# Kernel tuning notes

Measured on AMD Instinct MI355X. Metric: run time of the kernel, lower is better.

Reference implementation:

```python
import jax, jax.numpy as jnp
import numpy as np
from jax import lax

# Model hyperparameters (from module source: D_state=2, Expand=1; mamba-ssm defaults)
B_, C_, H_, W_ = 16, 128, 96, 96
D_MODEL = C_
D_INNER = 1 * D_MODEL          # expand = 1
D_STATE = 2
DT_RANK = (D_MODEL + 15) // 16  # ceil(d_model/16) = 8
D_CONV = 4
OUT_C = 128
LN_EPS = 1e-5


def setup_inputs() -> dict:
    key = jax.random.key(0)
    ks = jax.random.split(key, 10)
    s = 0.02
    x = jax.random.normal(ks[0], (B_, C_, H_, W_), dtype=jnp.float32)
    in_proj_w = jax.random.normal(ks[1], (2 * D_INNER, D_MODEL), dtype=jnp.float32) * s
    conv_w = jax.random.normal(ks[2], (D_INNER, 1, D_CONV), dtype=jnp.float32) * s
    conv_b = jnp.zeros((D_INNER,), dtype=jnp.float32)
    x_proj_w = jax.random.normal(ks[3], (DT_RANK + 2 * D_STATE, D_INNER), dtype=jnp.float32) * s
    dt_proj_w = jax.random.normal(ks[4], (D_INNER, DT_RANK), dtype=jnp.float32) * s
    # softplus^{-1}(0.01) so initial dt ~ 0.01 (standard mamba init)
    dt_proj_b = jnp.full((D_INNER,), float(np.log(np.expm1(0.01))), dtype=jnp.float32)
    A_log = jnp.log(jnp.broadcast_to(jnp.arange(1, D_STATE + 1, dtype=jnp.float32), (D_INNER, D_STATE)))
    D_param = jnp.ones((D_INNER,), dtype=jnp.float32)
    out_proj_w = jax.random.normal(ks[5], (OUT_C, D_INNER), dtype=jnp.float32) * s
    ln_gamma = jnp.ones((OUT_C,), dtype=jnp.float32)
    ln_beta = jnp.zeros((OUT_C,), dtype=jnp.float32)
    return {
        "x": x, "in_proj_w": in_proj_w, "conv_w": conv_w, "conv_b": conv_b,
        "x_proj_w": x_proj_w, "dt_proj_w": dt_proj_w, "dt_proj_b": dt_proj_b,
        "A_log": A_log, "D_param": D_param, "out_proj_w": out_proj_w,
        "ln_gamma": ln_gamma, "ln_beta": ln_beta,
    }


def _ssm_cha(x, in_proj_w, conv_w, conv_b, x_proj_w, dt_proj_w, dt_proj_b,
             A_log, D_param, out_proj_w, ln_gamma, ln_beta):
    b, c, h, w = x.shape
    L = h * w
    tokens = x.transpose(0, 2, 3, 1).reshape(b, L, c)  # [b, L, d_model]

    # in_proj -> (x_in, z)
    xz = jnp.einsum("bld,ed->ble", tokens, in_proj_w)  # [b, L, 2*d_inner]
    x_in, z = jnp.split(xz, 2, axis=-1)

    # causal depthwise conv1d over L, then SiLU
    xc = x_in.transpose(0, 2, 1)  # [b, d_inner, L]
    xc = lax.conv_general_dilated(
        xc, conv_w, window_strides=(1,), padding=[(D_CONV - 1, 0)],
        dimension_numbers=("NCH", "OIH", "NCH"), feature_group_count=D_INNER,
    ) + conv_b[None, :, None]
    x_in = jax.nn.silu(xc).transpose(0, 2, 1)  # [b, L, d_inner]

    # x_proj -> (dt, B, C)
    x_dbl = jnp.einsum("bld,ed->ble", x_in, x_proj_w)
    dt = x_dbl[..., :DT_RANK]
    Bc = x_dbl[..., DT_RANK:DT_RANK + D_STATE]         # [b, L, n]
    Cc = x_dbl[..., DT_RANK + D_STATE:]                # [b, L, n]
    dt = jax.nn.softplus(jnp.einsum("blr,dr->bld", dt, dt_proj_w) + dt_proj_b)

    # selective scan (diagonal A) via associative scan over L
    A = -jnp.exp(A_log)                                # [d_inner, n]
    dA = jnp.exp(dt[..., None] * A)                    # [b, L, d_inner, n]
    dBx = dt[..., None] * Bc[:, :, None, :] * x_in[..., None]

    def combine(e1, e2):
        a1, b1 = e1
        a2, b2 = e2
        return a1 * a2, a2 * b1 + b2

    _, hstate = lax.associative_scan(combine, (dA, dBx), axis=1)  # [b, L, d, n]
    y = jnp.sum(hstate * Cc[:, :, None, :], axis=-1) + D_param * x_in  # [b, L, d]

    y = y * jax.nn.silu(z)
    out = jnp.einsum("bld,od->blo", y, out_proj_w)     # [b, L, out_c]

    # LayerNorm over out_c
    mu = jnp.mean(out, axis=-1, keepdims=True)
    var = jnp.mean(jnp.square(out - mu), axis=-1, keepdims=True)
    out = (out - mu) * lax.rsqrt(var + LN_EPS) * ln_gamma + ln_beta

    return out.reshape(b, h, w, OUT_C).transpose(0, 3, 1, 2)


def reference(x, in_proj_w, conv_w, conv_b, x_proj_w, dt_proj_w, dt_proj_b,
              A_log, D_param, out_proj_w, ln_gamma, ln_beta):
    return _ssm_cha(x, in_proj_w, conv_w, conv_b, x_proj_w, dt_proj_w, dt_proj_b,
                    A_log, D_param, out_proj_w, ln_gamma, ln_beta)
```

## Files before the change

### kernel.cpp

```cpp
#include <hip/hip_runtime.h>
#include <hip/hip_bf16.h>

#define B_N 16
#define L_N 9216
#define LT64 144

typedef __attribute__((ext_vector_type(8))) short short8;
typedef __attribute__((ext_vector_type(4))) float floatx4;

__device__ __forceinline__ float bfu(unsigned short u) {
  return __uint_as_float(((unsigned int)u) << 16);
}
__device__ __forceinline__ unsigned short fbf(float f) {
  __hip_bfloat16 h = __float2bfloat16(f);
  return *(unsigned short*)&h;
}

__global__ __launch_bounds__(256) void k_prep(const float* __restrict__ w1,
                                              const float* __restrict__ w2,
                                              __hip_bfloat16* __restrict__ w1bt,
                                              __hip_bfloat16* __restrict__ w2bt) {
  int i = blockIdx.x * 256 + threadIdx.x;
  if (i < 256 * 128) w1bt[i] = __float2bfloat16(w1[i]);
  if (i < 128 * 128) w2bt[i] = __float2bfloat16(w2[i]);
}

__global__ __launch_bounds__(256) void k_xt(const float* __restrict__ x,
                                            __hip_bfloat16* __restrict__ xt) {
  __shared__ float xs[128][65];
  int blk = blockIdx.x, b = blk / LT64, lt = blk % LT64, l0 = lt * 64;
  int t = threadIdx.x;
  const float* xb = x + (size_t)b * 128 * L_N;
#pragma unroll
  for (int i = 0; i < 8; ++i) {
    int idx = t + i * 256;
    int c = idx >> 4, f4 = idx & 15;
    float4 v = *(const float4*)(xb + (size_t)c * L_N + l0 + f4 * 4);
    xs[c][f4 * 4 + 0] = v.x; xs[c][f4 * 4 + 1] = v.y;
    xs[c][f4 * 4 + 2] = v.z; xs[c][f4 * 4 + 3] = v.w;
  }
  __syncthreads();
  __hip_bfloat16* xtb = xt + ((size_t)b * L_N + l0) * 128;
#pragma unroll
  for (int i = 0; i < 16; ++i) {
    int idx = t + i * 256;
    int cp = idx & 63, l = idx >> 6;
    __hip_bfloat162 u;
    u.x = __float2bfloat16(xs[2 * cp][l]);
    u.y = __float2bfloat16(xs[2 * cp + 1][l]);
    *(__hip_bfloat162*)(xtb + (size_t)l * 128 + 2 * cp) = u;
  }
}

__global__ __launch_bounds__(256) void k_inproj_conv(
    const __hip_bfloat16* __restrict__ xt, const __hip_bfloat16* __restrict__ w1bt,
    const float* __restrict__ cw, const float* __restrict__ cb,
    const float* __restrict__ xpw,
    __hip_bfloat16* __restrict__ xinb, __hip_bfloat16* __restrict__ zb,
    float* __restrict__ xdblT) {
  __shared__ __align__(16) char smem[16384];
  __hip_bfloat16* xs = (__hip_bfloat16*)smem;
  float (*red)[12][64] = (float(*)[12][64])smem;
  __shared__ float cvs[128][68];
  int blk = blockIdx.x, b = blk / LT64, lt = blk % LT64, l0 = lt * 64;
  int t = threadIdx.x;
  const __hip_bfloat16* src = xt + ((size_t)b * L_N + l0) * 128;
#pragma unroll
  for (int i = 0; i < 4; ++i) {
    int idx = t + i * 256;
    int row = idx >> 4, ch = idx & 15;
    uint4 v = *(const uint4*)(src + idx * 8);
    *(uint4*)&xs[row * 128 + ((ch ^ (row & 7)) * 8)] = v;
  }
  int lane = t & 63, wv = t >> 6;
  int col = lane & 15, quad = lane >> 4;
  int e0 = wv * 64;
  short8 afr[4][4];
  const __hip_bfloat16* wb = w1bt + (size_t)(e0 + col) * 128 + quad * 8;
#pragma unroll
  for (int mi = 0; mi < 4; ++mi)
#pragma unroll
    for (int ks = 0; ks < 4; ++ks)
      afr[mi][ks] = *(const short8*)(wb + mi * 16 * 128 + ks * 32);
  floatx4 vzero = {0.f, 0.f, 0.f, 0.f};
  floatx4 acc[4][4];
#pragma unroll
  for (int mi = 0; mi < 4; ++mi)
#pragma unroll
    for (int ni = 0; ni < 4; ++ni) acc[mi][ni] = vzero;
  __syncthreads();
#pragma unroll
  for (int ks = 0; ks < 4; ++ks) {
    short8 bfr[4];
#pragma unroll
    for (int ni = 0; ni < 4; ++ni) {
      int row = ni * 16 + col;
      bfr[ni] = *(const short8*)&xs[row * 128 + (((ks * 4 + quad) ^ (row & 7)) * 8)];
    }
#pragma unroll
    for (int mi = 0; mi < 4; ++mi)
#pragma unroll
      for (int ni = 0; ni < 4; ++ni)
        acc[mi][ni] = __builtin_amdgcn_mfma_f32_16x16x32_bf16(afr[mi][ks], bfr[ni], acc[mi][ni], 0, 0, 0);
  }
  if (t < 128) {
    float s0 = 0.f, s1 = 0.f, s2 = 0.f;
    if (lt > 0) {
      const __hip_bfloat16* wr = w1bt + (size_t)t * 128;
      const __hip_bfloat16* x0r = xt + ((size_t)b * L_N + l0 - 3) * 128;
#pragma unroll
      for (int c8 = 0; c8 < 16; ++c8) {
        short8 wc = *(const short8*)(wr + c8 * 8);
        short8 xa = *(const short8*)(x0r + c8 * 8);
        short8 xb2 = *(const short8*)(x0r + 128 + c8 * 8);
        short8 xc = *(const short8*)(x0r + 256 + c8 * 8);
#pragma unroll
        for (int e = 0; e < 8; ++e) {
          float wf = bfu((unsigned short)wc[e]);
          s0 += wf * bfu((unsigned short)xa[e]);
          s1 += wf * bfu((unsigned short)xb2[e]);
          s2 += wf * bfu((unsigned short)xc[e]);
        }
      }
    }
    cvs[t][0] = s0; cvs[t][1] = s1; cvs[t][2] = s2;
  }
  if (wv < 2) {
#pragma unroll
    for (int mi = 0; mi < 4; ++mi)
#pragma unroll
      for (int r = 0; r < 4; ++r) {
        int d = e0 + mi * 16 + quad * 4 + r;
#pragma unroll
        for (int ni = 0; ni < 4; ++ni) cvs[d][3 + ni * 16 + col] = acc[mi][ni][r];
      }
  } else {
    __hip_bfloat16* zbase = zb + ((size_t)b * 128 + (e0 - 128)) * L_N + l0;
#pragma unroll
    for (int mi = 0; mi < 4; ++mi)
#pragma unroll
      for (int r = 0; r < 4; ++r) {
        int dr = mi * 16 + quad * 4 + r;
#pragma unroll
        for (int ni = 0; ni < 4; ++ni)
          zbase[(size_t)dr * L_N + ni * 16 + col] = __float2bfloat16(acc[mi][ni][r]);
      }
  }
  __syncthreads();
  float part[12];
#pragma unroll
  for (int m = 0; m < 12; ++m) part[m] = 0.f;
  for (int dd = 0; dd < 32; ++dd) {
    int d = wv * 32 + dd;
    float v = cb[d] + cw[d * 4 + 0] * cvs[d][lane] + cw[d * 4 + 1] * cvs[d][lane + 1]
                    + cw[d * 4 + 2] * cvs[d][lane + 2] + cw[d * 4 + 3] * cvs[d][lane + 3];
    v = v / (1.f + __expf(-v));
    xinb[((size_t)b * 128 + d) * L_N + l0 + lane] = __float2bfloat16(v);
#pragma unroll
    for (int m = 0; m < 12; ++m) part[m] += xpw[m * 128 + d] * v;
  }
#pragma unroll
  for (int m = 0; m < 12; ++m) red[wv][m][lane] = part[m];
  __syncthreads();
  for (int idx = t; idx < 12 * 64; idx += 256) {
    int m = idx >> 6, l = idx & 63;
    float s = red[0][m][l] + red[1][m][l] + red[2][m][l] + red[3][m][l];
    xdblT[((size_t)b * 12 + m) * L_N + l0 + l] = s;
  }
}

__global__ __launch_bounds__(256) void k_scan(
    const float* __restrict__ xdblT, const float* __restrict__ dtw,
    const float* __restrict__ dtb, const float* __restrict__ alog,
    const float* __restrict__ dpar,
    const __hip_bfloat16* __restrict__ xinb, const __hip_bfloat16* __restrict__ zb,
    __hip_bfloat16* __restrict__ yb) {
  __shared__ float agg[4][4];
  __shared__ float carry[2];
  int blk = blockIdx.x, b = blk >> 7, d = blk & 127;
  int t = threadIdx.x, lane = t & 63, wv = t >> 6;
  float A0 = -__expf(alog[2 * d]), A1 = -__expf(alog[2 * d + 1]);
  float Dv = dpar[d], dtbv = dtb[d];
  float w[8];
#pragma unroll
  for (int i = 0; i < 8; ++i) w[i] = dtw[d * 8 + i];
  if (t == 0) { carry[0] = 0.f; carry[1] = 0.f; }
  __syncthreads();
  const float* xdT = xdblT + (size_t)b * 12 * L_N;
  const unsigned short* xi = (const unsigned short*)xinb + ((size_t)b * 128 + d) * L_N;
  const unsigned short* zr = (const unsigned short*)zb + ((size_t)b * 128 + d) * L_N;
  unsigned short* yo = (unsigned short*)yb + ((size_t)b * 128 + d) * L_N;
  for (int it = 0; it < 9; ++it) {
    int lb = it * 1024 + t * 4;
    float4 q[12];
#pragma unroll
    for (int m = 0; m < 12; ++m) q[m] = *(const float4*)(xdT + (size_t)m * L_N + lb);
    ushort4 xu = *(const ushort4*)(xi + lb);
    ushort4 zu = *(const ushort4*)(zr + lb);
    float xv[4] = {bfu(xu.x), bfu(xu.y), bfu(xu.z), bfu(xu.w)};
    float zv[4] = {bfu(zu.x), bfu(zu.y), bfu(zu.z), bfu(zu.w)};
    float A0p[4], X0p[4], A1p[4], X1p[4];
#pragma unroll
    for (int j = 0; j < 4; ++j) {
      float dtp = dtbv;
#pragma unroll
      for (int m = 0; m < 8; ++m) dtp += w[m] * ((const float*)&q[m])[j];
      float dt = (dtp > 15.f) ? dtp : __logf(1.f + __expf(dtp));
      float a0 = __expf(dt * A0), a1 = __expf(dt * A1);
      float dtx = dt * xv[j];
      float x0 = dtx * ((const float*)&q[8])[j];
      float x1 = dtx * ((const float*)&q[9])[j];
      if (j == 0) { A0p[0] = a0; X0p[0] = x0; A1p[0] = a1; X1p[0] = x1; }
      else {
        A0p[j] = a0 * A0p[j - 1]; X0p[j] = a0 * X0p[j - 1] + x0;
        A1p[j] = a1 * A1p[j - 1]; X1p[j] = a1 * X1p[j - 1] + x1;
      }
    }
    float wA0 = A0p[3], wX0 = X0p[3], wA1 = A1p[3], wX1 = X1p[3];
#pragma unroll
    for (int off = 1; off < 64; off <<= 1) {
      float pA0 = __shfl_up(wA0, off, 64), pX0 = __shfl_up(wX0, off, 64);
      float pA1 = __shfl_up(wA1, off, 64), pX1 = __shfl_up(wX1, off, 64);
      if (lane >= off) {
        wX0 += wA0 * pX0; wA0 *= pA0;
        wX1 += wA1 * pX1; wA1 *= pA1;
      }
    }
    if (lane == 63) { agg[wv][0] = wA0; agg[wv][1] = wX0; agg[wv][2] = wA1; agg[wv][3] = wX1; }
    float eA0 = __shfl_up(wA0, 1, 64), eX0 = __shfl_up(wX0, 1, 64);
    float eA1 = __shfl_up(wA1, 1, 64), eX1 = __shfl_up(wX1, 1, 64);
    if (lane == 0) { eA0 = 1.f; eX0 = 0.f; eA1 = 1.f; eX1 = 0.f; }
    __syncthreads();
    float h0 = carry[0], h1 = carry[1];
    for (int jw = 0; jw < wv; ++jw) {
      h0 = agg[jw][0] * h0 + agg[jw][1];
      h1 = agg[jw][2] * h1 + agg[jw][3];
    }
    h0 = eA0 * h0 + eX0;
    h1 = eA1 * h1 + eX1;
    __syncthreads();
    if (t == 255) { carry[0] = A0p[3] * h0 + X0p[3]; carry[1] = A1p[3] * h1 + X1p[3]; }
    ushort4 yu;
    unsigned short* yp = (unsigned short*)&yu;
#pragma unroll
    for (int j = 0; j < 4; ++j) {
      float hh0 = A0p[j] * h0 + X0p[j];
      float hh1 = A1p[j] * h1 + X1p[j];
      float y = hh0 * ((const float*)&q[10])[j] + hh1 * ((const float*)&q[11])[j] + Dv * xv[j];
      y *= zv[j] / (1.f + __expf(-zv[j]));
      yp[j] = fbf(y);
    }
    *(ushort4*)(yo + lb) = yu;
  }
}

__global__ __launch_bounds__(256) void k_outln(
    const __hip_bfloat16* __restrict__ yb, const __hip_bfloat16* __restrict__ w2bt,
    const float* __restrict__ gam, const float* __restrict__ bet,
    float* __restrict__ out) {
  __shared__ unsigned short st[128][68];
  __shared__ __hip_bfloat16 yts[64 * 128];
  __shared__ float red_s[4][64], red_q[4][64];
  __shared__ float gs[128], bs[128];
  int blk = blockIdx.x, b = blk / LT64, lt = blk % LT64, l0 = lt * 64;
  int t = threadIdx.x;
  if (t < 128) { gs[t] = gam[t]; bs[t] = bet[t]; }
  const unsigned short* ybb = (const unsigned short*)yb + (size_t)b * 128 * L_N + l0;
#pragma unroll
  for (int i = 0; i < 8; ++i) {
    int idx = t + i * 256;
    int dd = idx >> 4, l4 = (idx & 15) * 4;
    ushort4 v = *(const ushort4*)(ybb + (size_t)dd * L_N + l4);
    *(ushort4*)&st[dd][l4] = v;
  }
  __syncthreads();
#pragma unroll
  for (int p = 0; p < 4; ++p) {
    int gi = t + p * 256;
    int l = gi & 63, ch = gi >> 6;
    short8 c;
#pragma unroll
    for (int j = 0; j < 8; ++j) c[j] = (short)st[ch * 8 + j][l];
    *(short8*)&yts[l * 128 + ((ch ^ (l & 7)) * 8)] = c;
  }
  int lane = t & 63, wv = t >> 6;
  int col = lane & 15, quad = lane >> 4;
  int o0 = wv * 32;
  short8 afr[2][4];
#pragma unroll
  for (int mi = 0; mi < 2; ++mi)
#pragma unroll
    for (int ks = 0; ks < 4; ++ks)
      afr[mi][ks] = *(const short8*)(w2bt + (size_t)(o0 + mi * 16 + col) * 128 + ks * 32 + quad * 8);
  floatx4 vzero = {0.f, 0.f, 0.f, 0.f};
  floatx4 acc[2][4];
#pragma unroll
  for (int mi = 0; mi < 2; ++mi)
#pragma unroll
    for (int ni = 0; ni < 4; ++ni) acc[mi][ni] = vzero;
  __syncthreads();
#pragma unroll
  for (int ks = 0; ks < 4; ++ks) {
    short8 bfr[4];
#pragma unroll
    for (int ni = 0; ni < 4; ++ni) {
      int row = ni * 16 + col;
      bfr[ni] = *(const short8*)&yts[row * 128 + (((ks * 4 + quad) ^ (row & 7)) * 8)];
    }
#pragma unroll
    for (int mi = 0; mi < 2; ++mi)
#pragma unroll
      for (int ni = 0; ni < 4; ++ni)
        acc[mi][ni] = __builtin_amdgcn_mfma_f32_16x16x32_bf16(afr[mi][ks], bfr[ni], acc[mi][ni], 0, 0, 0);
  }
  float s[4], q[4];
#pragma unroll
  for (int ni = 0; ni < 4; ++ni) {
    float ss = 0.f, qq = 0.f;
#pragma unroll
    for (int mi = 0; mi < 2; ++mi)
#pragma unroll
      for (int r = 0; r < 4; ++r) {
        float v = acc[mi][ni][r];
        ss += v; qq += v * v;
      }
    ss += __shfl_xor(ss, 16, 64); ss += __shfl_xor(ss, 32, 64);
    qq += __shfl_xor(qq, 16, 64); qq += __shfl_xor(qq, 32, 64);
    s[ni] = ss; q[ni] = qq;
  }
  if (quad == 0) {
#pragma unroll
    for (int ni = 0; ni < 4; ++ni) {
      red_s[wv][ni * 16 + col] = s[ni];
      red_q[wv][ni * 16 + col] = q[ni];
    }
  }
  __syncthreads();
  float mu[4], rstd[4];
#pragma unroll
  for (int ni = 0; ni < 4; ++ni) {
    int li = ni * 16 + col;
    float ts = red_s[0][li] + red_s[1][li] + red_s[2][li] + red_s[3][li];
    float tq = red_q[0][li] + red_q[1][li] + red_q[2][li] + red_q[3][li];
    float m = ts * (1.f / 128.f);
    float var = tq * (1.f / 128.f) - m * m;
    mu[ni] = m;
    rstd[ni] = rsqrtf(var + 1e-5f);
  }
  float* ob = out + (size_t)b * 128 * L_N;
#pragma unroll
  for (int mi = 0; mi < 2; ++mi)
#pragma unroll
    for (int r = 0; r < 4; ++r) {
      int o = o0 + mi * 16 + quad * 4 + r;
      float g = gs[o], bb = bs[o];
#pragma unroll
      for (int ni = 0; ni < 4; ++ni)
        ob[(size_t)o * L_N + l0 + ni * 16 + col] = (acc[mi][ni][r] - mu[ni]) * rstd[ni] * g + bb;
    }
}

extern "C" void kernel_launch(void* const* d_in, const int* in_sizes, int n_in,
                              void* d_out, int out_size, void* d_ws, size_t ws_size,
                              hipStream_t stream) {
  const float* x    = (const float*)d_in[0];
  const float* w1   = (const float*)d_in[1];
  const float* cw   = (const float*)d_in[2];
  const float* cb   = (const float*)d_in[3];
  const float* xpw  = (const float*)d_in[4];
  const float* dtw  = (const float*)d_in[5];
  const float* dtb  = (const float*)d_in[6];
  const float* alog = (const float*)d_in[7];
  const float* dpar = (const float*)d_in[8];
  const float* w2   = (const float*)d_in[9];
  const float* gam  = (const float*)d_in[10];
  const float* bet  = (const float*)d_in[11];
  float* out = (float*)d_out;

  float* ws = (float*)d_ws;
  const size_t NBL = (size_t)B_N * 128 * L_N;
  float* xdblT = ws;
  __hip_bfloat16* xt   = (__hip_bfloat16*)(ws + (size_t)B_N * 12 * L_N);
  __hip_bfloat16* xinb = xt + NBL;
  __hip_bfloat16* zb   = xinb + NBL;
  __hip_bfloat16* yb   = zb + NBL;
  __hip_bfloat16* w1bt = yb + NBL;
  __hip_bfloat16* w2bt = w1bt + 256 * 128;

  k_prep<<<128, 256, 0, stream>>>(w1, w2, w1bt, w2bt);
  k_xt<<<B_N * LT64, 256, 0, stream>>>(x, xt);
  k_inproj_conv<<<B_N * LT64, 256, 0, stream>>>(xt, w1bt, cw, cb, xpw, xinb, zb, xdblT);
  k_scan<<<B_N * 128, 256, 0, stream>>>(xdblT, dtw, dtb, alog, dpar, xinb, zb, yb);
  k_outln<<<B_N * LT64, 256, 0, stream>>>(yb, w2bt, gam, bet, out);
}
```

Before: 316.5 us.

## Fuse input transpose into in-projection kernel, reading NCHW fp32 directly

Removes the separate k_xt kernel that transposed x to token-major bf16. The in-projection kernel now loads the fp32 NCHW tile plus an 8-token halo, converts it to bf16 in shared memory and transposes it into the swizzled MFMA layout. The conv halo dot products now read from that shared tile instead of global memory. This drops one launch and a full bf16 write and read of x, at the cost of more shared memory per block, which may lower occupancy.

```diff
diff --git a/kernel.cpp b/kernel.cpp
--- a/kernel.cpp
+++ b/kernel.cpp
@@ -25,53 +25,34 @@
   if (i < 128 * 128) w2bt[i] = __float2bfloat16(w2[i]);
 }
 
-__global__ __launch_bounds__(256) void k_xt(const float* __restrict__ x,
-                                            __hip_bfloat16* __restrict__ xt) {
-  __shared__ float xs[128][65];
-  int blk = blockIdx.x, b = blk / LT64, lt = blk % LT64, l0 = lt * 64;
-  int t = threadIdx.x;
-  const float* xb = x + (size_t)b * 128 * L_N;
-#pragma unroll
-  for (int i = 0; i < 8; ++i) {
-    int idx = t + i * 256;
-    int c = idx >> 4, f4 = idx & 15;
-    float4 v = *(const float4*)(xb + (size_t)c * L_N + l0 + f4 * 4);
-    xs[c][f4 * 4 + 0] = v.x; xs[c][f4 * 4 + 1] = v.y;
-    xs[c][f4 * 4 + 2] = v.z; xs[c][f4 * 4 + 3] = v.w;
-  }
-  __syncthreads();
-  __hip_bfloat16* xtb = xt + ((size_t)b * L_N + l0) * 128;
-#pragma unroll
-  for (int i = 0; i < 16; ++i) {
-    int idx = t + i * 256;
-    int cp = idx & 63, l = idx >> 6;
-    __hip_bfloat162 u;
-    u.x = __float2bfloat16(xs[2 * cp][l]);
-    u.y = __float2bfloat16(xs[2 * cp + 1][l]);
-    *(__hip_bfloat162*)(xtb + (size_t)l * 128 + 2 * cp) = u;
-  }
-}
-
 __global__ __launch_bounds__(256) void k_inproj_conv(
-    const __hip_bfloat16* __restrict__ xt, const __hip_bfloat16* __restrict__ w1bt,
+    const float* __restrict__ x, const __hip_bfloat16* __restrict__ w1bt,
     const float* __restrict__ cw, const float* __restrict__ cb,
     const float* __restrict__ xpw,
     __hip_bfloat16* __restrict__ xinb, __hip_bfloat16* __restrict__ zb,
     float* __restrict__ xdblT) {
-  __shared__ __align__(16) char smem[16384];
-  __hip_bfloat16* xs = (__hip_bfloat16*)smem;
-  float (*red)[12][64] = (float(*)[12][64])smem;
-  __shared__ float cvs[128][68];
+  __shared__ __align__(16) char smem1[16384];
+  __shared__ __align__(16) char smem2[34816];
+  __hip_bfloat16* xs = (__hip_bfloat16*)smem1;
+  float (*red)[12][64] = (float(*)[12][64])smem1;
+  unsigned short (*st)[73] = (unsigned short(*)[73])smem2;
+  float (*cvs)[68] = (float(*)[68])smem2;
+
   int blk = blockIdx.x, b = blk / LT64, lt = blk % LT64, l0 = lt * 64;
   int t = threadIdx.x;
-  const __hip_bfloat16* src = xt + ((size_t)b * L_N + l0) * 128;
-#pragma unroll
-  for (int i = 0; i < 4; ++i) {
+
+  const float* xb = x + (size_t)b * 128 * L_N + (l0 - 8);
+#pragma unroll
+  for (int i = 0; i < 9; ++i) {
     int idx = t + i * 256;
-    int row = idx >> 4, ch = idx & 15;
-    uint4 v = *(const uint4*)(src + idx * 8);
-    *(uint4*)&xs[row * 128 + ((ch ^ (row & 7)) * 8)] = v;
-  }
+    int c = idx / 18, q = idx % 18;
+    float4 v;
+    if (lt == 0 && q < 2) { v.x = 0.f; v.y = 0.f; v.z = 0.f; v.w = 0.f; }
+    else v = *(const float4*)(xb + (size_t)c * L_N + q * 4);
+    st[c][q * 4 + 0] = fbf(v.x); st[c][q * 4 + 1] = fbf(v.y);
+    st[c][q * 4 + 2] = fbf(v.z); st[c][q * 4 + 3] = fbf(v.w);
+  }
+
   int lane = t & 63, wv = t >> 6;
   int col = lane & 15, quad = lane >> 4;
   int e0 = wv * 64;
@@ -82,6 +63,19 @@
 #pragma unroll
     for (int ks = 0; ks < 4; ++ks)
       afr[mi][ks] = *(const short8*)(wb + mi * 16 * 128 + ks * 32);
+
+  __syncthreads();
+
+#pragma unroll
+  for (int p = 0; p < 4; ++p) {
+    int gi = t + p * 256;
+    int l = gi >> 4, ch = gi & 15;
+    short8 cc;
+#pragma unroll
+    for (int j = 0; j < 8; ++j) cc[j] = (short)st[ch * 8 + j][8 + l];
+    *(short8*)&xs[l * 128 + ((ch ^ (l & 7)) * 8)] = cc;
+  }
+
   floatx4 vzero = {0.f, 0.f, 0.f, 0.f};
   floatx4 acc[4][4];
 #pragma unroll
@@ -89,6 +83,7 @@
 #pragma unroll
     for (int ni = 0; ni < 4; ++ni) acc[mi][ni] = vzero;
   __syncthreads();
+
 #pragma unroll
   for (int ks = 0; ks < 4; ++ks) {
     short8 bfr[4];
@@ -103,28 +98,38 @@
       for (int ni = 0; ni < 4; ++ni)
         acc[mi][ni] = __builtin_amdgcn_mfma_f32_16x16x32_bf16(afr[mi][ks], bfr[ni], acc[mi][ni], 0, 0, 0);
   }
-  if (t < 128) {
-    float s0 = 0.f, s1 = 0.f, s2 = 0.f;
-    if (lt > 0) {
-      const __hip_bfloat16* wr = w1bt + (size_t)t * 128;
-      const __hip_bfloat16* x0r = xt + ((size_t)b * L_N + l0 - 3) * 128;
-#pragma unroll
-      for (int c8 = 0; c8 < 16; ++c8) {
-        short8 wc = *(const short8*)(wr + c8 * 8);
-        short8 xa = *(const short8*)(x0r + c8 * 8);
-        short8 xb2 = *(const short8*)(x0r + 128 + c8 * 8);
-        short8 xc = *(const short8*)(x0r + 256 + c8 * 8);
-#pragma unroll
-        for (int e = 0; e < 8; ++e) {
-          float wf = bfu((unsigned short)wc[e]);
-          s0 += wf * bfu((unsigned short)xa[e]);
-          s1 += wf * bfu((unsigned short)xb2[e]);
-          s2 += wf * bfu((unsigned short)xc[e]);
-        }
-      }
-    }
-    cvs[t][0] = s0; cvs[t][1] = s1; cvs[t][2] = s2;
-  }
+
+  float s0 = 0.f, s1 = 0.f, s2 = 0.f;
+  if (t < 128 && lt > 0) {
+    const __hip_bfloat16* wr = w1bt + (size_t)t * 128;
+#pragma unroll
+    for (int c8 = 0; c8 < 16; ++c8) {
+      short8 wc = *(const short8*)(wr + c8 * 8);
+#pragma unroll
+      for (int e = 0; e < 8; ++e) {
+        int c = c8 * 8 + e;
+        float wf = bfu((unsigned short)wc[e]);
+        s0 += wf * bfu(st[c][5]);
+        s1 += wf * bfu(st[c][6]);
+        s2 += wf * bfu(st[c][7]);
+      }
+    }
+  }
+  if (wv >= 2) {
+    __hip_bfloat16* zbase = zb + ((size_t)b * 128 + (e0 - 128)) * L_N + l0;
+#pragma unroll
+    for (int mi = 0; mi < 4; ++mi)
+#pragma unroll
+      for (int r = 0; r < 4; ++r) {
+        int dr = mi * 16 + quad * 4 + r;
+#pragma unroll
+        for (int ni = 0; ni < 4; ++ni)
+          zbase[(size_t)dr * L_N + ni * 16 + col] = __float2bfloat16(acc[mi][ni][r]);
+      }
+  }
+  __syncthreads();
+
+  if (t < 128) { cvs[t][0] = s0; cvs[t][1] = s1; cvs[t][2] = s2; }
   if (wv < 2) {
 #pragma unroll
     for (int mi = 0; mi < 4; ++mi)
@@ -134,19 +139,9 @@
 #pragma unroll
         for (int ni = 0; ni < 4; ++ni) cvs[d][3 + ni * 16 + col] = acc[mi][ni][r];
       }
-  } else {
-    __hip_bfloat16* zbase = zb + ((size_t)b * 128 + (e0 - 128)) * L_N + l0;
-#pragma unroll
-    for (int mi = 0; mi < 4; ++mi)
-#pragma unroll
-      for (int r = 0; r < 4; ++r) {
-        int dr = mi * 16 + quad * 4 + r;
-#pragma unroll
-        for (int ni = 0; ni < 4; ++ni)
-          zbase[(size_t)dr * L_N + ni * 16 + col] = __float2bfloat16(acc[mi][ni][r]);
-      }
-  }
-  __syncthreads();
+  }
+  __syncthreads();
+
   float part[12];
 #pragma unroll
   for (int m = 0; m < 12; ++m) part[m] = 0.f;
@@ -380,16 +375,14 @@
   float* ws = (float*)d_ws;
   const size_t NBL = (size_t)B_N * 128 * L_N;
   float* xdblT = ws;
-  __hip_bfloat16* xt   = (__hip_bfloat16*)(ws + (size_t)B_N * 12 * L_N);
-  __hip_bfloat16* xinb = xt + NBL;
+  __hip_bfloat16* xinb = (__hip_bfloat16*)(ws + (size_t)B_N * 12 * L_N);
   __hip_bfloat16* zb   = xinb + NBL;
   __hip_bfloat16* yb   = zb + NBL;
   __hip_bfloat16* w1bt = yb + NBL;
   __hip_bfloat16* w2bt = w1bt + 256 * 128;
 
   k_prep<<<128, 256, 0, stream>>>(w1, w2, w1bt, w2bt);
-  k_xt<<<B_N * LT64, 256, 0, stream>>>(x, xt);
-  k_inproj_conv<<<B_N * LT64, 256, 0, stream>>>(xt, w1bt, cw, cb, xpw, xinb, zb, xdblT);
+  k_inproj_conv<<<B_N * LT64, 256, 0, stream>>>(x, w1bt, cw, cb, xpw, xinb, zb, xdblT);
   k_scan<<<B_N * 128, 256, 0, stream>>>(xdblT, dtw, dtb, alog, dpar, xinb, zb, yb);
   k_outln<<<B_N * LT64, 256, 0, stream>>>(yb, w2bt, gam, bet, out);
 }
```

New measurement: 321.6 us. Within noise of the previous version (+1.6%).
